# Kernel tuning notes

Hardware: AMD Instinct MI355X
Metric: run time of the kernel (lower is better)

Reference implementation:

```python
import jax, jax.numpy as jnp
import numpy as np

BN_EPS = 1e-5


def setup_inputs() -> dict:
    key = jax.random.key(0)
    ks = jax.random.split(key, 5)
    b, c, h, w = 4, 256, 64, 64
    pre = jax.random.normal(ks[0], (b, c, h, w), dtype=jnp.float32)
    cur = jax.random.normal(ks[1], (b, c, h, w), dtype=jnp.float32)
    # 1x1 conv weight stored as [out_ch, in_ch] (kernel is 1x1)
    W = jax.random.normal(ks[2], (256, 2 * c), dtype=jnp.float32) * (1.0 / np.sqrt(2 * c))
    b_conv = jax.random.normal(ks[3], (256,), dtype=jnp.float32) * 0.01
    gamma = jnp.ones((256,), dtype=jnp.float32)
    beta = jnp.zeros((256,), dtype=jnp.float32)
    run_mean = jnp.zeros((256,), dtype=jnp.float32)
    run_var = jnp.ones((256,), dtype=jnp.float32)
    alpha = jnp.full((1,), 0.25, dtype=jnp.float32)  # PReLU single shared slope
    return {"pre": pre, "cur": cur, "W": W, "b_conv": b_conv, "gamma": gamma,
            "beta": beta, "run_mean": run_mean, "run_var": run_var, "alpha": alpha}


def reference(pre, cur, W, b_conv, gamma, beta, run_mean, run_var, alpha):
    b, c, h, w = cur.shape
    hw = h * w
    pre_a = pre.reshape(b, c, hw)            # [b, c, hw]
    cur_a = cur.reshape(b, c, hw)            # [b, c, hw]
    # scores[b, i, j] = sum_c pre[b,c,i] * cur[b,c,j]
    scores = jnp.einsum('bci,bcj->bij', pre_a, cur_a)
    attn = jax.nn.softmax(scores * (c ** -0.5), axis=-1)   # [b, hw, hw]
    # feat[b, c, i] = sum_j attn[b,i,j] * cur[b,c,j]
    feat = jnp.einsum('bij,bcj->bci', attn, cur_a)          # [b, c, hw]
    x = jnp.concatenate([feat, cur_a], axis=1).reshape(b, 2 * c, h, w)
    # 1x1 conv
    y = jnp.einsum('bchw,oc->bohw', x, W) + b_conv[None, :, None, None]
    # BatchNorm2d (inference: running stats)
    inv = gamma * jax.lax.rsqrt(run_var + BN_EPS)
    y = y * inv[None, :, None, None] + (beta - run_mean * inv)[None, :, None, None]
    # PReLU (single shared parameter)
    a = alpha[0]
    return jnp.where(y >= 0, y, a * y)
```

## Files before the change

kernel.cpp:

```cpp
#include <hip/hip_runtime.h>
#include <hip/hip_bf16.h>
#include <math.h>

#define HWX 4096
#define CCH 256
#define NB  4

typedef __attribute__((ext_vector_type(8))) short short8;
typedef __attribute__((ext_vector_type(4))) short short4v;
typedef __attribute__((ext_vector_type(4))) float f32x4;
typedef __attribute__((ext_vector_type(2))) float f32x2;

#define WS_QT 0ull
#define WS_KT 8388608ull
#define WS_V  16777216ull
#define WS_W  25165824ull
#define WS_FT 25427968ull
#define WS_PO 33816576ull

__device__ __forceinline__ short f2bf(float f) {
  union { float f; unsigned u; } a; a.f = f;
  unsigned r = a.u + 0x7FFFu + ((a.u >> 16) & 1u);
  return (short)(r >> 16);
}

__device__ __forceinline__ float bf2f(short s) {
  union { unsigned u; float f; } a;
  a.u = ((unsigned)(unsigned short)s) << 16;
  return a.f;
}

__device__ __forceinline__ short f2bf_rn(float f) {
  __hip_bfloat16 h = __float2bfloat16(f);
  return *reinterpret_cast<short*>(&h);
}

__device__ __forceinline__ f32x4 mfma16(short8 a, short8 b, f32x4 c) {
  return __builtin_amdgcn_mfma_f32_16x16x32_bf16(a, b, c, 0, 0, 0);
}

__device__ __forceinline__ void gload16(const void* g, void* l) {
  __builtin_amdgcn_global_load_lds(
      (const __attribute__((address_space(1))) unsigned int*)g,
      (__attribute__((address_space(3))) unsigned int*)l, 16, 0, 0);
}

__global__ __launch_bounds__(256) void prep_qkv(const float* __restrict__ pre,
                                                const float* __restrict__ cur,
                                                char* __restrict__ ws) {
  __shared__ short ldsT[256 * 36];
  const int tid = threadIdx.x;
  const int b  = blockIdx.x >> 7;
  const int jt = blockIdx.x & 127;
  const int j0 = jt * 32;
  const float* preB = pre + (size_t)b * CCH * HWX + j0;
  const float* curB = cur + (size_t)b * CCH * HWX + j0;
  char* vout = ws + WS_V  + (size_t)(b * 128 + jt) * 16384;
  char* kout = ws + WS_KT + (size_t)(b * 128 + jt) * 16384;
  char* qout = ws + WS_QT + (size_t)(b * 128 + jt) * 16384;

  short v[32];
  {
    const float* p = curB + (size_t)tid * HWX;
#pragma unroll
    for (int k = 0; k < 8; ++k) {
      f32x4 f = *(const f32x4*)(p + k * 4);
      v[k*4+0] = f2bf(f[0]); v[k*4+1] = f2bf(f[1]);
      v[k*4+2] = f2bf(f[2]); v[k*4+3] = f2bf(f[3]);
    }
  }
#pragma unroll
  for (int k = 0; k < 4; ++k) {
    short8 o8;
#pragma unroll
    for (int e = 0; e < 8; ++e) o8[e] = v[k * 8 + e];
    *(short8*)(vout + ((tid * 64 + k * 16) ^ ((tid & 7) << 4))) = o8;
  }
#pragma unroll
  for (int j = 0; j < 32; ++j) ldsT[tid * 36 + j] = v[j];
  __syncthreads();
  {
    const int j = tid >> 3, m = tid & 7;
#pragma unroll
    for (int k = 0; k < 4; ++k) {
      short8 o8;
#pragma unroll
      for (int e = 0; e < 8; ++e) o8[e] = ldsT[(m * 32 + k * 8 + e) * 36 + j];
      *(short8*)(kout + ((j * 512 + m * 64 + k * 16) ^ ((j & 7) << 4))) = o8;
    }
  }
  __syncthreads();
  {
    const float* p = preB + (size_t)tid * HWX;
#pragma unroll
    for (int k = 0; k < 8; ++k) {
      f32x4 f = *(const f32x4*)(p + k * 4);
      v[k*4+0] = f2bf(f[0]); v[k*4+1] = f2bf(f[1]);
      v[k*4+2] = f2bf(f[2]); v[k*4+3] = f2bf(f[3]);
    }
  }
#pragma unroll
  for (int j = 0; j < 32; ++j) ldsT[tid * 36 + j] = v[j];
  __syncthreads();
  {
    const int j = tid >> 3, m = tid & 7;
#pragma unroll
    for (int k = 0; k < 4; ++k) {
      short8 o8;
#pragma unroll
      for (int e = 0; e < 8; ++e) o8[e] = ldsT[(m * 32 + k * 8 + e) * 36 + j];
      *(short8*)(qout + ((j * 512 + m * 64 + k * 16) ^ ((j & 7) << 4))) = o8;
    }
  }
}

__global__ __launch_bounds__(256) void prep_w(const float* __restrict__ Wm,
                                              char* __restrict__ ws) {
  const int sl = blockIdx.x;
  const int o  = threadIdx.x;
  char* out = ws + WS_W + (size_t)sl * 32768;
  const float* src = Wm + (size_t)o * 512 + sl * 64;
  short tmp[64];
#pragma unroll
  for (int k = 0; k < 16; ++k) {
    f32x4 f = *(const f32x4*)(src + k * 4);
    tmp[k*4+0] = f2bf(f[0]); tmp[k*4+1] = f2bf(f[1]);
    tmp[k*4+2] = f2bf(f[2]); tmp[k*4+3] = f2bf(f[3]);
  }
#pragma unroll
  for (int k = 0; k < 8; ++k) {
    short8 o8;
#pragma unroll
    for (int e = 0; e < 8; ++e) o8[e] = tmp[k * 8 + e];
    *(short8*)(out + ((o * 128 + k * 16) ^ ((o & 7) << 4))) = o8;
  }
}

__global__ __launch_bounds__(256, 2) void attn_db4(char* __restrict__ ws) {
  __shared__ __align__(16) char smem[75776];
  const int tid = threadIdx.x, lane = tid & 63, wv = tid >> 6;
  const int g = lane >> 4, l15 = lane & 15;
  const int p = blockIdx.x;
  const int L = (p & 7) * 64 + (p >> 3);
  const int b = L >> 7, s = (L >> 5) & 3, it = L & 31;
  const int i0 = it * 128;
  const int NT = 32;
  const char* qimg  = ws + WS_QT + (size_t)(b * 128 + it * 4) * 16384;
  const char* kbase = ws + WS_KT + (size_t)(b * 128 + s * NT) * 16384;
  const char* vbase = ws + WS_V  + (size_t)(b * 128 + s * NT) * 16384;

#pragma unroll
  for (int k = 0; k < 16; ++k)
    gload16(qimg + k * 4096 + tid * 16, smem + k * 4096 + tid * 16);
  __syncthreads();
  short8 qf[2][8];
  {
    const char* qt = smem + wv * 16384;
#pragma unroll
    for (int qsub = 0; qsub < 2; ++qsub)
#pragma unroll
      for (int kb = 0; kb < 8; ++kb)
        qf[qsub][kb] = *(const short8*)(qt + (qsub * 16 + l15) * 512 +
                                        ((kb * 64 + g * 16) ^ ((l15 & 7) << 4)));
  }
  __syncthreads();

  f32x4 acc[2][16];
#pragma unroll
  for (int qsub = 0; qsub < 2; ++qsub)
#pragma unroll
    for (int nt = 0; nt < 16; ++nt) acc[qsub][nt] = (f32x4){0.f, 0.f, 0.f, 0.f};
  f32x4 accl[2];
  accl[0] = (f32x4){0.f, 0.f, 0.f, 0.f};
  accl[1] = (f32x4){0.f, 0.f, 0.f, 0.f};
  const float SL2E = 1.4426950408889634f / 16.0f;
  short8 ones;
#pragma unroll
  for (int e = 0; e < 8; ++e) ones[e] = (short)16256;

#pragma unroll
  for (int k = 0; k < 4; ++k) {
    gload16(kbase + k * 4096 + tid * 16, smem + k * 4096 + tid * 16);
    gload16(vbase + k * 4096 + tid * 16, smem + 16384 + k * 4096 + tid * 16);
  }
  __syncthreads();

  short* pw = (short*)(smem + 65536 + wv * 2560);
  int cur = 0;
  for (int t = 0; t < NT; ++t) {
    if (t + 1 < NT) {
      const char* ks = kbase + (size_t)(t + 1) * 16384;
      const char* vs = vbase + (size_t)(t + 1) * 16384;
      char* dst = smem + (cur ^ 1) * 32768 + tid * 16;
#pragma unroll
      for (int k = 0; k < 4; ++k) {
        gload16(ks + k * 4096 + tid * 16, dst + k * 4096);
        gload16(vs + k * 4096 + tid * 16, dst + 16384 + k * 4096);
      }
    }
    const char* bk = smem + cur * 32768;
    const char* bv = bk + 16384;
    f32x4 s00 = (f32x4){0.f,0.f,0.f,0.f}, s01 = (f32x4){0.f,0.f,0.f,0.f};
    f32x4 s10 = (f32x4){0.f,0.f,0.f,0.f}, s11 = (f32x4){0.f,0.f,0.f,0.f};
    __builtin_amdgcn_s_setprio(1);
#pragma unroll
    for (int kb = 0; kb < 8; ++kb) {
      const int co = (kb * 64 + g * 16) ^ ((l15 & 7) << 4);
      short8 k0 = *(const short8*)(bk + l15 * 512 + co);
      short8 k1 = *(const short8*)(bk + (l15 + 16) * 512 + co);
      s00 = mfma16(qf[0][kb], k0, s00);
      s01 = mfma16(qf[0][kb], k1, s01);
      s10 = mfma16(qf[1][kb], k0, s10);
      s11 = mfma16(qf[1][kb], k1, s11);
    }
    __builtin_amdgcn_s_setprio(0);
#pragma unroll
    for (int r = 0; r < 4; ++r) {
      pw[(g * 4 + r) * 40 + l15]           = f2bf_rn(exp2f(fmaf(s00[r], SL2E, -16.0f)));
      pw[(g * 4 + r) * 40 + 16 + l15]      = f2bf_rn(exp2f(fmaf(s01[r], SL2E, -16.0f)));
      pw[(16 + g * 4 + r) * 40 + l15]      = f2bf_rn(exp2f(fmaf(s10[r], SL2E, -16.0f)));
      pw[(16 + g * 4 + r) * 40 + 16 + l15] = f2bf_rn(exp2f(fmaf(s11[r], SL2E, -16.0f)));
    }
    short8 pf0 = *(const short8*)((const char*)pw + l15 * 80 + g * 16);
    short8 pf1 = *(const short8*)((const char*)pw + (16 + l15) * 80 + g * 16);
    __builtin_amdgcn_s_setprio(1);
    accl[0] = mfma16(pf0, ones, accl[0]);
    accl[1] = mfma16(pf1, ones, accl[1]);
#pragma unroll
    for (int nt = 0; nt < 16; ++nt) {
      const int c = nt * 16 + l15;
      short8 vf = *(const short8*)(bv + ((c * 64 + g * 16) ^ ((c & 7) << 4)));
      acc[0][nt] = mfma16(pf0, vf, acc[0][nt]);
      acc[1][nt] = mfma16(pf1, vf, acc[1][nt]);
    }
    __builtin_amdgcn_s_setprio(0);
    __syncthreads();
    cur ^= 1;
  }

  short* po = (short*)(ws + WS_PO) + (size_t)(s * NB + b) * CCH * HWX;
#pragma unroll
  for (int qsub = 0; qsub < 2; ++qsub)
#pragma unroll
    for (int nt = 0; nt < 16; ++nt) {
      const int c = nt * 16 + l15;
      short4v o4;
#pragma unroll
      for (int r = 0; r < 4; ++r) o4[r] = f2bf_rn(acc[qsub][nt][r]);
      *(short4v*)(po + (size_t)c * HWX + i0 + wv * 32 + qsub * 16 + g * 4) = o4;
    }
  if (l15 == 0) {
    short* pl = (short*)(ws + WS_PO + 4ull * 8388608ull) +
                (size_t)(s * NB + b) * HWX + i0 + wv * 32 + g * 4;
    short4v a4, b4;
#pragma unroll
    for (int r = 0; r < 4; ++r) { a4[r] = f2bf_rn(accl[0][r]); b4[r] = f2bf_rn(accl[1][r]); }
    *(short4v*)pl = a4;
    *(short4v*)(pl + 16) = b4;
  }
}

template <int S>
__global__ __launch_bounds__(128, 2) void attn_sb(char* __restrict__ ws) {
  __shared__ __align__(16) char smem[37888];
  const int tid = threadIdx.x, lane = tid & 63, wv = tid >> 6;
  const int g = lane >> 4, l15 = lane & 15;
  const int p = blockIdx.x;
  const int NT = 128 / S;
  int b, s, it;
  if (S == 2) {
    const int L = (p & 7) * 64 + (p >> 3);
    b = L >> 7; s = (L >> 6) & 1; it = L & 63;
  } else {
    const int L = (p & 7) * 32 + (p >> 3);
    b = L >> 6; s = 0; it = L & 63;
  }
  const int i0 = it * 64;
  const char* qimg  = ws + WS_QT + (size_t)(b * 128 + it * 2) * 16384;
  const char* kbase = ws + WS_KT + (size_t)(b * 128 + s * NT) * 16384;
  const char* vbase = ws + WS_V  + (size_t)(b * 128 + s * NT) * 16384;

#pragma unroll
  for (int k = 0; k < 16; ++k)
    gload16(qimg + k * 2048 + tid * 16, smem + k * 2048 + tid * 16);
  __syncthreads();
  short8 qf[2][8];
  {
    const char* qt = smem + wv * 16384;
#pragma unroll
    for (int qsub = 0; qsub < 2; ++qsub)
#pragma unroll
      for (int kb = 0; kb < 8; ++kb)
        qf[qsub][kb] = *(const short8*)(qt + (qsub * 16 + l15) * 512 +
                                        ((kb * 64 + g * 16) ^ ((l15 & 7) << 4)));
  }
  __syncthreads();

  f32x4 acc[2][16];
#pragma unroll
  for (int qsub = 0; qsub < 2; ++qsub)
#pragma unroll
    for (int nt = 0; nt < 16; ++nt) acc[qsub][nt] = (f32x4){0.f, 0.f, 0.f, 0.f};
  f32x4 accl[2];
  accl[0] = (f32x4){0.f, 0.f, 0.f, 0.f};
  accl[1] = (f32x4){0.f, 0.f, 0.f, 0.f};
  const float SL2E = 1.4426950408889634f / 16.0f;
  short8 ones;
#pragma unroll
  for (int e = 0; e < 8; ++e) ones[e] = (short)16256;

#pragma unroll
  for (int k = 0; k < 8; ++k) {
    gload16(kbase + k * 2048 + tid * 16, smem + k * 2048 + tid * 16);
    gload16(vbase + k * 2048 + tid * 16, smem + 16384 + k * 2048 + tid * 16);
  }
  __syncthreads();

  short* pw = (short*)(smem + 32768 + wv * 2560);
  for (int t = 0; t < NT; ++t) {
    const char* bk = smem;
    const char* bv = smem + 16384;
    f32x4 s00 = (f32x4){0.f,0.f,0.f,0.f}, s01 = (f32x4){0.f,0.f,0.f,0.f};
    f32x4 s10 = (f32x4){0.f,0.f,0.f,0.f}, s11 = (f32x4){0.f,0.f,0.f,0.f};
    __builtin_amdgcn_s_setprio(1);
#pragma unroll
    for (int kb = 0; kb < 8; ++kb) {
      const int co = (kb * 64 + g * 16) ^ ((l15 & 7) << 4);
      short8 k0 = *(const short8*)(bk + l15 * 512 + co);
      short8 k1 = *(const short8*)(bk + (l15 + 16) * 512 + co);
      s00 = mfma16(qf[0][kb], k0, s00);
      s01 = mfma16(qf[0][kb], k1, s01);
      s10 = mfma16(qf[1][kb], k0, s10);
      s11 = mfma16(qf[1][kb], k1, s11);
    }
    __builtin_amdgcn_s_setprio(0);
#pragma unroll
    for (int r = 0; r < 4; ++r) {
      pw[(g * 4 + r) * 40 + l15]           = f2bf_rn(exp2f(fmaf(s00[r], SL2E, -16.0f)));
      pw[(g * 4 + r) * 40 + 16 + l15]      = f2bf_rn(exp2f(fmaf(s01[r], SL2E, -16.0f)));
      pw[(16 + g * 4 + r) * 40 + l15]      = f2bf_rn(exp2f(fmaf(s10[r], SL2E, -16.0f)));
      pw[(16 + g * 4 + r) * 40 + 16 + l15] = f2bf_rn(exp2f(fmaf(s11[r], SL2E, -16.0f)));
    }
    short8 pf0 = *(const short8*)((const char*)pw + l15 * 80 + g * 16);
    short8 pf1 = *(const short8*)((const char*)pw + (16 + l15) * 80 + g * 16);
    __builtin_amdgcn_s_setprio(1);
    accl[0] = mfma16(pf0, ones, accl[0]);
    accl[1] = mfma16(pf1, ones, accl[1]);
#pragma unroll
    for (int nt = 0; nt < 16; ++nt) {
      const int c = nt * 16 + l15;
      short8 vf = *(const short8*)(bv + ((c * 64 + g * 16) ^ ((c & 7) << 4)));
      acc[0][nt] = mfma16(pf0, vf, acc[0][nt]);
      acc[1][nt] = mfma16(pf1, vf, acc[1][nt]);
    }
    __builtin_amdgcn_s_setprio(0);
    __syncthreads();
    if (t + 1 < NT) {
      const char* ks = kbase + (size_t)(t + 1) * 16384;
      const char* vs = vbase + (size_t)(t + 1) * 16384;
#pragma unroll
      for (int k = 0; k < 8; ++k) {
        gload16(ks + k * 2048 + tid * 16, smem + k * 2048 + tid * 16);
        gload16(vs + k * 2048 + tid * 16, smem + 16384 + k * 2048 + tid * 16);
      }
    }
    __syncthreads();
  }

  short* po = (short*)(ws + WS_PO) + (size_t)(s * NB + b) * CCH * HWX;
#pragma unroll
  for (int qsub = 0; qsub < 2; ++qsub)
#pragma unroll
    for (int nt = 0; nt < 16; ++nt) {
      const int c = nt * 16 + l15;
      short4v o4;
#pragma unroll
      for (int r = 0; r < 4; ++r) o4[r] = f2bf_rn(acc[qsub][nt][r]);
      *(short4v*)(po + (size_t)c * HWX + i0 + wv * 32 + qsub * 16 + g * 4) = o4;
    }
  if (l15 == 0) {
    short* pl = (short*)(ws + WS_PO + (size_t)S * 8388608ull) +
                (size_t)(s * NB + b) * HWX + i0 + wv * 32 + g * 4;
    short4v a4, b4;
#pragma unroll
    for (int r = 0; r < 4; ++r) { a4[r] = f2bf_rn(accl[0][r]); b4[r] = f2bf_rn(accl[1][r]); }
    *(short4v*)pl = a4;
    *(short4v*)(pl + 16) = b4;
  }
}

template <int S>
__global__ __launch_bounds__(256) void merge_feat(char* __restrict__ ws) {
  __shared__ float linv[32];
  __shared__ short ldsT[32 * 66];
  const int tid = threadIdx.x;
  const int p = blockIdx.x;
  const int L = (p & 7) * 64 + (p >> 3);
  const int b = L >> 7, it = L & 127, i0 = it * 32;
  const short* po = (const short*)(ws + WS_PO);
  const short* pl = (const short*)(ws + WS_PO + (size_t)S * 8388608ull);
  if (tid < 32) {
    float l = 0.0f;
#pragma unroll
    for (int s = 0; s < S; ++s)
      l += bf2f(pl[(size_t)(s * NB + b) * HWX + i0 + tid]);
    linv[tid] = 1.0f / l;
  }
  __syncthreads();
  char* fout = ws + WS_FT + (size_t)(b * 128 + it) * 16384;
#pragma unroll
  for (int ch = 0; ch < 4; ++ch) {
    const int c = ch * 64 + (tid >> 2);
    const int qo = (tid & 3) * 8;
    float a[8];
#pragma unroll
    for (int e = 0; e < 8; ++e) a[e] = 0.0f;
#pragma unroll
    for (int s = 0; s < S; ++s) {
      short8 v8 = *(const short8*)(po + (size_t)(s * NB + b) * CCH * HWX +
                                   (size_t)c * HWX + i0 + qo);
#pragma unroll
      for (int e = 0; e < 8; ++e) a[e] += bf2f(v8[e]);
    }
#pragma unroll
    for (int e = 0; e < 8; ++e)
      ldsT[(qo + e) * 66 + (tid >> 2)] = f2bf(a[e] * linv[qo + e]);
    __syncthreads();
    {
      const int i = tid >> 3, m = tid & 7;
      short8 o8;
#pragma unroll
      for (int e = 0; e < 8; ++e) o8[e] = ldsT[i * 66 + m * 8 + e];
      *(short8*)(fout + ((i * 512 + ch * 128 + m * 16) ^ ((i & 7) << 4))) = o8;
    }
    __syncthreads();
  }
}

__global__ __launch_bounds__(256) void conv_mfma(const float* __restrict__ bconv,
                                                 const float* __restrict__ gamma,
                                                 const float* __restrict__ beta,
                                                 const float* __restrict__ rmean,
                                                 const float* __restrict__ rvar,
                                                 const float* __restrict__ alpha,
                                                 char* __restrict__ ws,
                                                 float* __restrict__ out) {
  __shared__ __align__(16) char smem[73728];
  const int tid = threadIdx.x, lane = tid & 63, wv = tid >> 6;
  const int g = lane >> 4, l15 = lane & 15;
  const int p = blockIdx.x;
  const int L = (p & 7) * 64 + (p >> 3);
  const int b = L >> 7, it = L & 127, i0 = it * 32;
  const char* wimg = ws + WS_W;
  const char* ft = ws + WS_FT + (size_t)(b * 128 + it) * 16384;
  const char* kt = ws + WS_KT + (size_t)(b * 128 + it) * 16384;

  f32x4 acc[4][2];
#pragma unroll
  for (int ot = 0; ot < 4; ++ot)
#pragma unroll
    for (int itt = 0; itt < 2; ++itt) acc[ot][itt] = (f32x4){0.f, 0.f, 0.f, 0.f};

  const int xi = wv * 8 + (lane >> 3), xw = (lane & 7) * 16;

#pragma unroll
  for (int k = 0; k < 8; ++k)
    gload16(wimg + wv * 8192 + k * 1024 + lane * 16,
            smem + wv * 8192 + k * 1024 + lane * 16);
  gload16(ft + xi * 512 + xw, smem + 65536 + wv * 1024 + lane * 16);
  __syncthreads();

  int cur = 0;
  for (int st = 0; st < 8; ++st) {
    if (st < 7) {
      const int sn = st + 1;
      const char* img = (sn < 4) ? ft : kt;
      const int coff = (sn & 3) * 128;
#pragma unroll
      for (int k = 0; k < 8; ++k)
        gload16(wimg + (size_t)sn * 32768 + wv * 8192 + k * 1024 + lane * 16,
                smem + (cur ^ 1) * 32768 + wv * 8192 + k * 1024 + lane * 16);
      gload16(img + xi * 512 + coff + xw,
              smem + 65536 + (cur ^ 1) * 4096 + wv * 1024 + lane * 16);
    }
    const char* wb = smem + cur * 32768;
    const char* xb = smem + 65536 + cur * 4096;
    short8 bx[2][2];
#pragma unroll
    for (int itt = 0; itt < 2; ++itt) {
      const int i = itt * 16 + l15;
#pragma unroll
      for (int kb = 0; kb < 2; ++kb)
        bx[itt][kb] = *(const short8*)(xb + i * 128 + ((kb * 64 + g * 16) ^ ((i & 7) << 4)));
    }
#pragma unroll
    for (int ot = 0; ot < 4; ++ot) {
      const int o = wv * 64 + ot * 16 + l15;
#pragma unroll
      for (int kb = 0; kb < 2; ++kb) {
        short8 aw = *(const short8*)(wb + o * 128 + ((kb * 64 + g * 16) ^ ((o & 7) << 4)));
#pragma unroll
        for (int itt = 0; itt < 2; ++itt)
          acc[ot][itt] = mfma16(aw, bx[itt][kb], acc[ot][itt]);
      }
    }
    __syncthreads();
    cur ^= 1;
  }

  const float a0 = alpha[0];
  float* outB = out + (size_t)b * CCH * HWX;
#pragma unroll
  for (int ot = 0; ot < 4; ++ot)
#pragma unroll
    for (int r = 0; r < 4; ++r) {
      const int o = wv * 64 + ot * 16 + g * 4 + r;
      const float inv = gamma[o] * rsqrtf(rvar[o] + 1e-5f);
      const float add = beta[o] - rmean[o] * inv + bconv[o] * inv;
#pragma unroll
      for (int itt = 0; itt < 2; ++itt) {
        float v = acc[ot][itt][r] * inv + add;
        v = (v >= 0.0f) ? v : a0 * v;
        outB[(size_t)o * HWX + i0 + itt * 16 + l15] = v;
      }
    }
}

__global__ __launch_bounds__(256) void legacy_attn(const float* __restrict__ pre,
                                                   const float* __restrict__ cur,
                                                   float* __restrict__ feat) {
  __shared__ __align__(16) char smem[43008];
  short* lds_q  = (short*)smem;
  short* lds_kT = (short*)smem;
  short* lds_v  = (short*)(smem + 16896);
  short* lds_p  = (short*)(smem + 37376);
  const int tid = threadIdx.x, lane = tid & 63, wv = tid >> 6;
  const int b = blockIdx.x >> 6, i0 = (blockIdx.x & 63) * 64;
  const float* preB = pre + (size_t)b * CCH * HWX;
  const float* curB = cur + (size_t)b * CCH * HWX;
  float* featB = feat + (size_t)b * CCH * HWX;
  {
    const int ib = (tid & 15) * 4, cbb = (tid >> 4) * 4;
#pragma unroll
    for (int p = 0; p < 4; ++p) {
      const int c = cbb + 64 * p;
      f32x4 f[4];
#pragma unroll
      for (int r = 0; r < 4; ++r)
        f[r] = *(const f32x4*)(preB + (size_t)(c + r) * HWX + i0 + ib);
#pragma unroll
      for (int e = 0; e < 4; ++e) {
        short4v s2;
        s2[0] = f2bf(f[0][e]); s2[1] = f2bf(f[1][e]);
        s2[2] = f2bf(f[2][e]); s2[3] = f2bf(f[3][e]);
        *(short4v*)(&lds_q[(ib + e) * 264 + c]) = s2;
      }
    }
  }
  __syncthreads();
  short8 qf[8];
  {
    const int r = wv * 16 + (lane & 15), ko = (lane >> 4) * 8;
#pragma unroll
    for (int kb = 0; kb < 8; ++kb)
      qf[kb] = *(const short8*)(&lds_q[r * 264 + kb * 32 + ko]);
  }
  f32x4 acc[16];
#pragma unroll
  for (int nt = 0; nt < 16; ++nt) acc[nt] = (f32x4){0.f, 0.f, 0.f, 0.f};
  float m_run[4], l_run[4];
#pragma unroll
  for (int r = 0; r < 4; ++r) { m_run[r] = -1e30f; l_run[r] = 0.0f; }
  const float SL2E = 1.4426950408889634f / 16.0f;
  for (int jt = 0; jt < 128; ++jt) {
    const int j0 = jt * 32;
    __syncthreads();
    {
      const int jb = (tid & 7) * 4, cbb = (tid >> 3) * 4;
#pragma unroll
      for (int p = 0; p < 2; ++p) {
        const int c = cbb + 128 * p;
        f32x4 f[4];
#pragma unroll
        for (int r = 0; r < 4; ++r)
          f[r] = *(const f32x4*)(curB + (size_t)(c + r) * HWX + j0 + jb);
#pragma unroll
        for (int r = 0; r < 4; ++r) {
          short4v s2;
          s2[0] = f2bf(f[r][0]); s2[1] = f2bf(f[r][1]);
          s2[2] = f2bf(f[r][2]); s2[3] = f2bf(f[r][3]);
          *(short4v*)(&lds_v[(c + r) * 40 + jb]) = s2;
        }
#pragma unroll
        for (int e = 0; e < 4; ++e) {
          short4v s2;
          s2[0] = f2bf(f[0][e]); s2[1] = f2bf(f[1][e]);
          s2[2] = f2bf(f[2][e]); s2[3] = f2bf(f[3][e]);
          *(short4v*)(&lds_kT[(jb + e) * 264 + c]) = s2;
        }
      }
    }
    __syncthreads();
    f32x4 s0 = (f32x4){0.f,0.f,0.f,0.f}, s1 = (f32x4){0.f,0.f,0.f,0.f};
    {
      const int jc = lane & 15, ko = (lane >> 4) * 8;
#pragma unroll
      for (int kb = 0; kb < 8; ++kb) {
        short8 k0 = *(const short8*)(&lds_kT[jc * 264 + kb * 32 + ko]);
        short8 k1 = *(const short8*)(&lds_kT[(jc + 16) * 264 + kb * 32 + ko]);
        s0 = mfma16(qf[kb], k0, s0);
        s1 = mfma16(qf[kb], k1, s1);
      }
    }
    float p0[4], p1[4], corr[4];
#pragma unroll
    for (int r = 0; r < 4; ++r) {
      float t = fmaxf(s0[r], s1[r]);
      t = fmaxf(t, __shfl_xor(t, 1)); t = fmaxf(t, __shfl_xor(t, 2));
      t = fmaxf(t, __shfl_xor(t, 4)); t = fmaxf(t, __shfl_xor(t, 8));
      const float mn = fmaxf(m_run[r], t * SL2E);
      corr[r] = exp2f(m_run[r] - mn);
      m_run[r] = mn;
      p0[r] = exp2f(s0[r] * SL2E - mn);
      p1[r] = exp2f(s1[r] * SL2E - mn);
      float rs = p0[r] + p1[r];
      rs += __shfl_xor(rs, 1); rs += __shfl_xor(rs, 2);
      rs += __shfl_xor(rs, 4); rs += __shfl_xor(rs, 8);
      l_run[r] = l_run[r] * corr[r] + rs;
    }
#pragma unroll
    for (int nt = 0; nt < 16; ++nt)
#pragma unroll
      for (int r = 0; r < 4; ++r) acc[nt][r] *= corr[r];
    {
      short* pw = lds_p + wv * 640;
      const int g = lane >> 4, jc = lane & 15;
#pragma unroll
      for (int r = 0; r < 4; ++r) {
        pw[(g * 4 + r) * 40 + jc]      = f2bf(p0[r]);
        pw[(g * 4 + r) * 40 + 16 + jc] = f2bf(p1[r]);
      }
    }
    {
      const int g = lane >> 4, rr = lane & 15;
      short8 pf = *(const short8*)(&lds_p[wv * 640 + rr * 40 + g * 8]);
#pragma unroll
      for (int nt = 0; nt < 16; ++nt) {
        short8 vf = *(const short8*)(&lds_v[(nt * 16 + rr) * 40 + g * 8]);
        acc[nt] = mfma16(pf, vf, acc[nt]);
      }
    }
  }
  {
    const int g = lane >> 4, jc = lane & 15;
    float rl[4];
#pragma unroll
    for (int r = 0; r < 4; ++r) rl[r] = 1.0f / l_run[r];
#pragma unroll
    for (int nt = 0; nt < 16; ++nt) {
      const int c = nt * 16 + jc;
#pragma unroll
      for (int r = 0; r < 4; ++r)
        featB[(size_t)c * HWX + i0 + wv * 16 + g * 4 + r] = acc[nt][r] * rl[r];
    }
  }
}

__global__ __launch_bounds__(256) void legacy_conv(const float* feat,
                                                   const float* __restrict__ cur,
                                                   const float* __restrict__ Wm,
                                                   const float* __restrict__ bconv,
                                                   const float* __restrict__ gamma,
                                                   const float* __restrict__ beta,
                                                   const float* __restrict__ rmean,
                                                   const float* __restrict__ rvar,
                                                   const float* __restrict__ alpha,
                                                   float* out) {
  __shared__ __align__(16) char smem[25600];
  short* lds_w = (short*)smem;
  short* lds_x = (short*)(smem + 20480);
  const int tid = threadIdx.x, lane = tid & 63, wv = tid >> 6;
  const int b = blockIdx.x >> 6, i0 = (blockIdx.x & 63) * 64;
  const float* featB = feat + (size_t)b * CCH * HWX;
  const float* curB  = cur  + (size_t)b * CCH * HWX;
  f32x4 acc[4][4];
#pragma unroll
  for (int ot = 0; ot < 4; ++ot)
#pragma unroll
    for (int it = 0; it < 4; ++it) acc[ot][it] = (f32x4){0.f, 0.f, 0.f, 0.f};
  for (int ks = 0; ks < 16; ++ks) {
    const int k0 = ks * 32;
    __syncthreads();
    {
      const int kq = (tid & 7) * 4, ob = tid >> 3;
#pragma unroll
      for (int p = 0; p < 8; ++p) {
        const int o = ob + 32 * p;
        f32x4 f = *(const f32x4*)(Wm + (size_t)o * 512 + k0 + kq);
        short4v s2;
        s2[0] = f2bf(f[0]); s2[1] = f2bf(f[1]); s2[2] = f2bf(f[2]); s2[3] = f2bf(f[3]);
        *(short4v*)(&lds_w[o * 40 + kq]) = s2;
      }
    }
    {
      const int i2 = (tid & 31) * 2, cc = ((tid >> 5) & 7) * 4;
      const float* basep = (k0 < 256) ? (featB + (size_t)(k0 + cc) * HWX)
                                      : (curB + (size_t)(k0 + cc - 256) * HWX);
      f32x2 f[4];
#pragma unroll
      for (int r = 0; r < 4; ++r)
        f[r] = *(const f32x2*)(basep + (size_t)r * HWX + i0 + i2);
#pragma unroll
      for (int e = 0; e < 2; ++e) {
        short4v s2;
        s2[0] = f2bf(f[0][e]); s2[1] = f2bf(f[1][e]);
        s2[2] = f2bf(f[2][e]); s2[3] = f2bf(f[3][e]);
        *(short4v*)(&lds_x[(i2 + e) * 40 + cc]) = s2;
      }
    }
    __syncthreads();
    {
      const int g = lane >> 4, rr = lane & 15;
      short8 af[4], bx[4];
#pragma unroll
      for (int ot = 0; ot < 4; ++ot)
        af[ot] = *(const short8*)(&lds_w[(wv * 64 + ot * 16 + rr) * 40 + g * 8]);
#pragma unroll
      for (int it = 0; it < 4; ++it)
        bx[it] = *(const short8*)(&lds_x[(it * 16 + rr) * 40 + g * 8]);
#pragma unroll
      for (int ot = 0; ot < 4; ++ot)
#pragma unroll
        for (int it = 0; it < 4; ++it)
          acc[ot][it] = mfma16(af[ot], bx[it], acc[ot][it]);
    }
  }
  const float a0 = alpha[0];
  const int g = lane >> 4, ic = lane & 15;
  float* outB = out + (size_t)b * CCH * HWX;
#pragma unroll
  for (int ot = 0; ot < 4; ++ot)
#pragma unroll
    for (int r = 0; r < 4; ++r) {
      const int o = wv * 64 + ot * 16 + g * 4 + r;
      const float inv = gamma[o] * rsqrtf(rvar[o] + 1e-5f);
      const float add = beta[o] - rmean[o] * inv + bconv[o] * inv;
#pragma unroll
      for (int it = 0; it < 4; ++it) {
        float v = acc[ot][it][r] * inv + add;
        v = (v >= 0.0f) ? v : a0 * v;
        outB[(size_t)o * HWX + i0 + it * 16 + ic] = v;
      }
    }
}

extern "C" void kernel_launch(void* const* d_in, const int* in_sizes, int n_in,
                              void* d_out, int out_size, void* d_ws, size_t ws_size,
                              hipStream_t stream) {
  (void)in_sizes; (void)n_in; (void)out_size;
  const float* pre   = (const float*)d_in[0];
  const float* cur   = (const float*)d_in[1];
  const float* Wm    = (const float*)d_in[2];
  const float* bconv = (const float*)d_in[3];
  const float* gamma = (const float*)d_in[4];
  const float* beta  = (const float*)d_in[5];
  const float* rmean = (const float*)d_in[6];
  const float* rvar  = (const float*)d_in[7];
  const float* alpha = (const float*)d_in[8];
  float* out = (float*)d_out;
  char* ws = (char*)d_ws;

  const size_t need4 = WS_PO + 4ull * (8388608ull + 32768ull);
  const size_t need2 = WS_PO + 2ull * (8388608ull + 32768ull);
  const size_t need1 = WS_PO + 1ull * (8388608ull + 32768ull);

  if (ws_size >= need1) {
    prep_qkv<<<dim3(512), dim3(256), 0, stream>>>(pre, cur, ws);
    prep_w<<<dim3(8), dim3(256), 0, stream>>>(Wm, ws);
    if (ws_size >= need4) {
      attn_db4<<<dim3(512), dim3(256), 0, stream>>>(ws);
      merge_feat<4><<<dim3(512), dim3(256), 0, stream>>>(ws);
    } else if (ws_size >= need2) {
      attn_sb<2><<<dim3(512), dim3(128), 0, stream>>>(ws);
      merge_feat<2><<<dim3(512), dim3(256), 0, stream>>>(ws);
    } else {
      attn_sb<1><<<dim3(256), dim3(128), 0, stream>>>(ws);
      merge_feat<1><<<dim3(512), dim3(256), 0, stream>>>(ws);
    }
    conv_mfma<<<dim3(512), dim3(256), 0, stream>>>(bconv, gamma, beta, rmean,
                                                   rvar, alpha, ws, out);
  } else {
    legacy_attn<<<dim3(256), dim3(256), 0, stream>>>(pre, cur, out);
    legacy_conv<<<dim3(256), dim3(256), 0, stream>>>(out, cur, Wm, bconv, gamma,
                                                     beta, rmean, rvar, alpha, out);
  }
}
```

Measured before the change: 137.7 us.

## Keep softmax probabilities in registers by permuting K layout and swapping MFMA operands

The QK^T MFMA operands are swapped so each lane's score accumulator lines up with the register layout the PV MFMA expects. Key rows are written in a permuted order in prep, and the conv stage reads with the inverse mapping. This removes the per-tile LDS round trip for the probability matrix (write, read back) and shrinks shared memory per block. It depends on the permutation being applied the same way in every consumer, which adds coupling and a risk of a mismatch.

Measured after the change: 124.6 us (median of 3 runs). 9.5% less time.

```diff
diff --git a/kernel.cpp b/kernel.cpp
--- a/kernel.cpp
+++ b/kernel.cpp
@@ -43,6 +43,10 @@
   __builtin_amdgcn_global_load_lds(
       (const __attribute__((address_space(1))) unsigned int*)g,
       (__attribute__((address_space(3))) unsigned int*)l, 16, 0, 0);
+}
+
+__device__ __forceinline__ int kt_invmap(int j) {
+  return (((j >> 2) & 1) << 4) | (((j >> 3) & 3) << 2) | (j & 3);
 }
 
 __global__ __launch_bounds__(256) void prep_qkv(const float* __restrict__ pre,
@@ -81,12 +85,13 @@
   __syncthreads();
   {
     const int j = tid >> 3, m = tid & 7;
+    const int a = kt_invmap(j);
 #pragma unroll
     for (int k = 0; k < 4; ++k) {
       short8 o8;
 #pragma unroll
       for (int e = 0; e < 8; ++e) o8[e] = ldsT[(m * 32 + k * 8 + e) * 36 + j];
-      *(short8*)(kout + ((j * 512 + m * 64 + k * 16) ^ ((j & 7) << 4))) = o8;
+      *(short8*)(kout + ((a * 512 + m * 64 + k * 16) ^ ((a & 7) << 4))) = o8;
     }
   }
   __syncthreads();
@@ -137,7 +142,7 @@
 }
 
 __global__ __launch_bounds__(256, 2) void attn_db4(char* __restrict__ ws) {
-  __shared__ __align__(16) char smem[75776];
+  __shared__ __align__(16) char smem[65536];
   const int tid = threadIdx.x, lane = tid & 63, wv = tid >> 6;
   const int g = lane >> 4, l15 = lane & 15;
   const int p = blockIdx.x;
@@ -185,7 +190,6 @@
   }
   __syncthreads();
 
-  short* pw = (short*)(smem + 65536 + wv * 2560);
   int cur = 0;
   for (int t = 0; t < NT; ++t) {
     if (t + 1 < NT) {
@@ -208,21 +212,20 @@
       const int co = (kb * 64 + g * 16) ^ ((l15 & 7) << 4);
       short8 k0 = *(const short8*)(bk + l15 * 512 + co);
       short8 k1 = *(const short8*)(bk + (l15 + 16) * 512 + co);
-      s00 = mfma16(qf[0][kb], k0, s00);
-      s01 = mfma16(qf[0][kb], k1, s01);
-      s10 = mfma16(qf[1][kb], k0, s10);
-      s11 = mfma16(qf[1][kb], k1, s11);
+      s00 = mfma16(k0, qf[0][kb], s00);
+      s01 = mfma16(k1, qf[0][kb], s01);
+      s10 = mfma16(k0, qf[1][kb], s10);
+      s11 = mfma16(k1, qf[1][kb], s11);
     }
     __builtin_amdgcn_s_setprio(0);
+    short8 pf0, pf1;
 #pragma unroll
     for (int r = 0; r < 4; ++r) {
-      pw[(g * 4 + r) * 40 + l15]           = f2bf_rn(exp2f(fmaf(s00[r], SL2E, -16.0f)));
-      pw[(g * 4 + r) * 40 + 16 + l15]      = f2bf_rn(exp2f(fmaf(s01[r], SL2E, -16.0f)));
-      pw[(16 + g * 4 + r) * 40 + l15]      = f2bf_rn(exp2f(fmaf(s10[r], SL2E, -16.0f)));
-      pw[(16 + g * 4 + r) * 40 + 16 + l15] = f2bf_rn(exp2f(fmaf(s11[r], SL2E, -16.0f)));
-    }
-    short8 pf0 = *(const short8*)((const char*)pw + l15 * 80 + g * 16);
-    short8 pf1 = *(const short8*)((const char*)pw + (16 + l15) * 80 + g * 16);
+      pf0[r]     = f2bf_rn(exp2f(fmaf(s00[r], SL2E, -16.0f)));
+      pf0[4 + r] = f2bf_rn(exp2f(fmaf(s01[r], SL2E, -16.0f)));
+      pf1[r]     = f2bf_rn(exp2f(fmaf(s10[r], SL2E, -16.0f)));
+      pf1[4 + r] = f2bf_rn(exp2f(fmaf(s11[r], SL2E, -16.0f)));
+    }
     __builtin_amdgcn_s_setprio(1);
     accl[0] = mfma16(pf0, ones, accl[0]);
     accl[1] = mfma16(pf1, ones, accl[1]);
@@ -262,7 +265,7 @@
 
 template <int S>
 __global__ __launch_bounds__(128, 2) void attn_sb(char* __restrict__ ws) {
-  __shared__ __align__(16) char smem[37888];
+  __shared__ __align__(16) char smem[32768];
   const int tid = threadIdx.x, lane = tid & 63, wv = tid >> 6;
   const int g = lane >> 4, l15 = lane & 15;
   const int p = blockIdx.x;
@@ -316,7 +319,6 @@
   }
   __syncthreads();
 
-  short* pw = (short*)(smem + 32768 + wv * 2560);
   for (int t = 0; t < NT; ++t) {
     const char* bk = smem;
     const char* bv = smem + 16384;
@@ -328,21 +330,20 @@
       const int co = (kb * 64 + g * 16) ^ ((l15 & 7) << 4);
       short8 k0 = *(const short8*)(bk + l15 * 512 + co);
       short8 k1 = *(const short8*)(bk + (l15 + 16) * 512 + co);
-      s00 = mfma16(qf[0][kb], k0, s00);
-      s01 = mfma16(qf[0][kb], k1, s01);
-      s10 = mfma16(qf[1][kb], k0, s10);
-      s11 = mfma16(qf[1][kb], k1, s11);
+      s00 = mfma16(k0, qf[0][kb], s00);
+      s01 = mfma16(k1, qf[0][kb], s01);
+      s10 = mfma16(k0, qf[1][kb], s10);
+      s11 = mfma16(k1, qf[1][kb], s11);
     }
     __builtin_amdgcn_s_setprio(0);
+    short8 pf0, pf1;
 #pragma unroll
     for (int r = 0; r < 4; ++r) {
-      pw[(g * 4 + r) * 40 + l15]           = f2bf_rn(exp2f(fmaf(s00[r], SL2E, -16.0f)));
-      pw[(g * 4 + r) * 40 + 16 + l15]      = f2bf_rn(exp2f(fmaf(s01[r], SL2E, -16.0f)));
-      pw[(16 + g * 4 + r) * 40 + l15]      = f2bf_rn(exp2f(fmaf(s10[r], SL2E, -16.0f)));
-      pw[(16 + g * 4 + r) * 40 + 16 + l15] = f2bf_rn(exp2f(fmaf(s11[r], SL2E, -16.0f)));
-    }
-    short8 pf0 = *(const short8*)((const char*)pw + l15 * 80 + g * 16);
-    short8 pf1 = *(const short8*)((const char*)pw + (16 + l15) * 80 + g * 16);
+      pf0[r]     = f2bf_rn(exp2f(fmaf(s00[r], SL2E, -16.0f)));
+      pf0[4 + r] = f2bf_rn(exp2f(fmaf(s01[r], SL2E, -16.0f)));
+      pf1[r]     = f2bf_rn(exp2f(fmaf(s10[r], SL2E, -16.0f)));
+      pf1[4 + r] = f2bf_rn(exp2f(fmaf(s11[r], SL2E, -16.0f)));
+    }
     __builtin_amdgcn_s_setprio(1);
     accl[0] = mfma16(pf0, ones, accl[0]);
     accl[1] = mfma16(pf1, ones, accl[1]);
@@ -489,9 +490,10 @@
 #pragma unroll
     for (int itt = 0; itt < 2; ++itt) {
       const int i = itt * 16 + l15;
+      const int ii = (st < 4) ? i : kt_invmap(i);
 #pragma unroll
       for (int kb = 0; kb < 2; ++kb)
-        bx[itt][kb] = *(const short8*)(xb + i * 128 + ((kb * 64 + g * 16) ^ ((i & 7) << 4)));
+        bx[itt][kb] = *(const short8*)(xb + ii * 128 + ((kb * 64 + g * 16) ^ ((ii & 7) << 4)));
     }
 #pragma unroll
     for (int ot = 0; ot < 4; ++ot) {
@@ -634,25 +636,25 @@
       for (int r = 0; r < 4; ++r) acc[nt][r] *= corr[r];
     {
       short* pw = lds_p + wv * 640;
-      const int g = lane >> 4, jc = lane & 15;
+      const int g2 = lane >> 4, jc = lane & 15;
 #pragma unroll
       for (int r = 0; r < 4; ++r) {
-        pw[(g * 4 + r) * 40 + jc]      = f2bf(p0[r]);
-        pw[(g * 4 + r) * 40 + 16 + jc] = f2bf(p1[r]);
+        pw[(g2 * 4 + r) * 40 + jc]      = f2bf(p0[r]);
+        pw[(g2 * 4 + r) * 40 + 16 + jc] = f2bf(p1[r]);
       }
     }
     {
-      const int g = lane >> 4, rr = lane & 15;
-      short8 pf = *(const short8*)(&lds_p[wv * 640 + rr * 40 + g * 8]);
+      const int g2 = lane >> 4, rr = lane & 15;
+      short8 pf = *(const short8*)(&lds_p[wv * 640 + rr * 40 + g2 * 8]);
 #pragma unroll
       for (int nt = 0; nt < 16; ++nt) {
-        short8 vf = *(const short8*)(&lds_v[(nt * 16 + rr) * 40 + g * 8]);
+        short8 vf = *(const short8*)(&lds_v[(nt * 16 + rr) * 40 + g2 * 8]);
         acc[nt] = mfma16(pf, vf, acc[nt]);
       }
     }
   }
   {
-    const int g = lane >> 4, jc = lane & 15;
+    const int g2 = lane >> 4, jc = lane & 15;
     float rl[4];
 #pragma unroll
     for (int r = 0; r < 4; ++r) rl[r] = 1.0f / l_run[r];
@@ -661,7 +663,7 @@
       const int c = nt * 16 + jc;
 #pragma unroll
       for (int r = 0; r < 4; ++r)
-        featB[(size_t)c * HWX + i0 + wv * 16 + g * 4 + r] = acc[nt][r] * rl[r];
+        featB[(size_t)c * HWX + i0 + wv * 16 + g2 * 4 + r] = acc[nt][r] * rl[r];
     }
   }
 }
```
